# Kernel tuning notes

Measured on AMD Instinct MI355X. Metric: run time of the kernel, lower is better.

Reference implementation:

```python
import jax, jax.numpy as jnp
import numpy as np

CHUNK = 64  # rows of `a` processed per step to bound the [chunk, N, d] abs-diff intermediate
TAIL_K = 4          # selection_tail_size
FAR_K = 64          # far_sample_count
PUSH_K = 4          # pushing_sample_size
HUBER_DELTA = 1.0   # torch.nn.HuberLoss default


def cdist_l1(a, b):
    # a: [M, d], b: [N, d] -> [M, N] Manhattan distances, computed in row chunks
    M, d = a.shape
    def f(a_chunk):  # [CHUNK, d] -> [CHUNK, N]
        return jnp.abs(a_chunk[:, None, :] - b[None, :, :]).sum(-1)
    return jax.lax.map(f, a.reshape(-1, CHUNK, d)).reshape(M, b.shape[0])


def smallest_k_mean(dists, k):
    # mean of the k smallest entries along last dim
    neg_vals, _ = jax.lax.top_k(-dists, k)
    return (-neg_vals).mean(-1)


def huber(x):
    # HuberLoss(pred=x, target=0), delta=1
    ax = jnp.abs(x)
    return jnp.where(ax < HUBER_DELTA, 0.5 * x * x, HUBER_DELTA * (ax - 0.5 * HUBER_DELTA))


def setup_inputs() -> dict:
    key = jax.random.key(0)
    k1, k2 = jax.random.split(key)
    space_samples = jax.random.normal(k1, (2048, 256), dtype=jnp.float32)
    latents = jax.random.normal(k2, (8192, 256), dtype=jnp.float32)
    return {"space_samples": space_samples, "latents": latents}


def reference(space_samples, latents):
    # space_samples: [M, d] drawn from latent_sampler; latents: [N, d]
    space_dists = cdist_l1(space_samples, latents)            # [M, N]
    tail_dists = smallest_k_mean(space_dists, TAIL_K)          # [M]
    far_inds = jax.lax.top_k(tail_dists, FAR_K)[1]             # [FAR_K]
    far_samples = space_samples[far_inds]                      # [FAR_K, d]
    empty_dists = cdist_l1(far_samples, latents)               # [FAR_K, N]
    close_dists = smallest_k_mean(empty_dists, PUSH_K)         # [FAR_K]
    return huber(close_dists).mean()
```

## Files before the change

### kernel.cpp

```cpp
#include <hip/hip_runtime.h>
#include <hip/hip_bf16.h>


static constexpr int M = 2048;
static constexpr int N = 8192;
static constexpr int KQ = 64;
static constexpr int ROWS_PER_BLK = 128;
static constexpr int COLS_PER_BLK = 128;
static constexpr int NCHUNK = N / COLS_PER_BLK;
static constexpr int SLD_RED = 132;

static constexpr float QS  = 21.0f;
static constexpr float QB  = 126.0f;
static constexpr float INV_QS = 1.0f / 21.0f;

__device__ __forceinline__ float med3f(float a, float b, float c) {
    return __builtin_amdgcn_fmed3f(a, b, c);
}

__device__ __forceinline__ void ins4(float d, float& s0, float& s1, float& s2, float& s3) {
    float n0 = fminf(s0, d);
    float n1 = med3f(s0, s1, d);
    float n2 = med3f(s1, s2, d);
    float n3 = med3f(s2, s3, d);
    s0 = n0; s1 = n1; s2 = n2; s3 = n3;
}

__device__ __forceinline__ unsigned int sad8(unsigned int a, unsigned int b, unsigned int c) {
#if __has_builtin(__builtin_amdgcn_sad_u8)
    return __builtin_amdgcn_sad_u8(a, b, c);
#else
    unsigned int d;
    asm("v_sad_u8 %0, %1, %2, %3" : "=v"(d) : "v"(a), "v"(b), "v"(c));
    return d;
#endif
}

__device__ __forceinline__ void gll16(const unsigned int* g, unsigned int* l) {
    __builtin_amdgcn_global_load_lds(
        (const __attribute__((address_space(1))) unsigned int*)g,
        (__attribute__((address_space(3))) unsigned int*)l, 16, 0, 0);
}

__device__ __forceinline__ unsigned int quant4(const float4 v) {
    const float y0 = fminf(fmaxf(fmaf(v.x, QS, QB), 0.0f), 255.0f);
    const float y1 = fminf(fmaxf(fmaf(v.y, QS, QB), 0.0f), 255.0f);
    const float y2 = fminf(fmaxf(fmaf(v.z, QS, QB), 0.0f), 255.0f);
    const float y3 = fminf(fmaxf(fmaf(v.w, QS, QB), 0.0f), 255.0f);
    const unsigned int b0 = (unsigned int)(int)rintf(y0);
    const unsigned int b1 = (unsigned int)(int)rintf(y1);
    const unsigned int b2 = (unsigned int)(int)rintf(y2);
    const unsigned int b3 = (unsigned int)(int)rintf(y3);
    return b0 | (b1 << 8) | (b2 << 16) | (b3 << 24);
}

__device__ __forceinline__ float huber_pos(float x) {
    const float ax = __builtin_fabsf(x);
    return (ax < 1.0f) ? (0.5f * x * x) : (ax - 0.5f);
}

__global__ __launch_bounds__(256)
void convert_kernel(const float* __restrict__ A, const float* __restrict__ B,
                    unsigned int* __restrict__ At, unsigned int* __restrict__ Bt) {
    __shared__ unsigned int lt[KQ * 65];
    const int tid = threadIdx.x;
    const bool isB = (blockIdx.x < N / 64);
    const float* src = isB ? B : A;
    unsigned int* dst = isB ? Bt : At;
    const int rows = isB ? N : M;
    const int r0 = (isB ? blockIdx.x : (blockIdx.x - N / 64)) * 64;

#pragma unroll
    for (int it = 0; it < 16; ++it) {
        const int qi = it * 256 + tid;
        const int row = qi >> 6;
        const int kq = qi & 63;
        const float4 v = *(const float4*)&src[(r0 + row) * 256 + 4 * kq];
        lt[kq * 65 + row] = quant4(v);
    }
    __syncthreads();
#pragma unroll
    for (int it = 0; it < 16; ++it) {
        const int wi = it * 256 + tid;
        const int row = wi & 63;
        const int kq = wi >> 6;
        dst[(size_t)kq * rows + r0 + row] = lt[kq * 65 + row];
    }
}

__global__ __launch_bounds__(256, 4)
void dist4_kernel(const unsigned int* __restrict__ At, const unsigned int* __restrict__ Bt,
                  float4* __restrict__ ws_dist) {
    __shared__ __align__(16) char smem[33792];
    unsigned int* bt = (unsigned int*)smem;
    const int tid = threadIdx.x;
    const int lane = tid & 63;
    const int w = __builtin_amdgcn_readfirstlane(tid >> 6);
    const int bx = blockIdx.x;
    const int by = blockIdx.y;
    const int rowBase = by * ROWS_PER_BLK;
    const int colBase = bx * COLS_PER_BLK;
    const int r0 = rowBase + w * 32;

#pragma unroll
    for (int it = 0; it < 8; ++it) {
        const int idx = it * 256 + tid;
        const int kq = idx >> 5;
        const int c4 = (idx & 31) * 4;
        gll16(&Bt[(size_t)kq * N + colBase + c4], bt + idx * 4);
    }

    unsigned int acc[32][2];
#pragma unroll
    for (int r = 0; r < 32; ++r) { acc[r][0] = 0u; acc[r][1] = 0u; }

    __syncthreads();

    const unsigned int* __restrict__ Arow = At + r0;
#pragma unroll 4
    for (int kq = 0; kq < KQ; ++kq) {
        const uint2 bb = *(const uint2*)&bt[kq * 128 + 2 * lane];
        const uint4* __restrict__ pa = (const uint4*)(Arow + (size_t)kq * M);
#pragma unroll
        for (int q = 0; q < 8; ++q) {
            const uint4 av = pa[q];
            acc[4*q+0][0] = sad8(av.x, bb.x, acc[4*q+0][0]);
            acc[4*q+0][1] = sad8(av.x, bb.y, acc[4*q+0][1]);
            acc[4*q+1][0] = sad8(av.y, bb.x, acc[4*q+1][0]);
            acc[4*q+1][1] = sad8(av.y, bb.y, acc[4*q+1][1]);
            acc[4*q+2][0] = sad8(av.z, bb.x, acc[4*q+2][0]);
            acc[4*q+2][1] = sad8(av.z, bb.y, acc[4*q+2][1]);
            acc[4*q+3][0] = sad8(av.w, bb.x, acc[4*q+3][0]);
            acc[4*q+3][1] = sad8(av.w, bb.y, acc[4*q+3][1]);
        }
    }

    float (*red)[SLD_RED] = (float (*)[SLD_RED])smem;
    __syncthreads();

#pragma unroll
    for (int p = 0; p < 2; ++p) {
        if ((w >> 1) == p) {
            const int rl = (w & 1) * 32;
#pragma unroll
            for (int r = 0; r < 32; ++r) {
                *(float2*)&red[rl + r][2 * lane] =
                    make_float2((float)acc[r][0] * INV_QS, (float)acc[r][1] * INV_QS);
            }
        }
        __syncthreads();
        {
            const int row = tid >> 2;
            const int seg = tid & 3;
            float s0 = 1e30f, s1 = 1e30f, s2 = 1e30f, s3 = 1e30f;
#pragma unroll
            for (int c = 0; c < 8; ++c) {
                const float4 v = *(const float4*)&red[row][seg * 4 + c * 16];
                ins4(v.x, s0, s1, s2, s3);
                ins4(v.y, s0, s1, s2, s3);
                ins4(v.z, s0, s1, s2, s3);
                ins4(v.w, s0, s1, s2, s3);
            }
#pragma unroll
            for (int lvl = 1; lvl <= 2; lvl <<= 1) {
                const float o0 = __shfl_xor(s0, lvl, 64);
                const float o1 = __shfl_xor(s1, lvl, 64);
                const float o2 = __shfl_xor(s2, lvl, 64);
                const float o3 = __shfl_xor(s3, lvl, 64);
                ins4(o0, s0, s1, s2, s3);
                ins4(o1, s0, s1, s2, s3);
                ins4(o2, s0, s1, s2, s3);
                ins4(o3, s0, s1, s2, s3);
            }
            if (seg == 0) {
                ws_dist[bx * M + rowBase + p * 64 + row] = make_float4(s0, s1, s2, s3);
            }
        }
        __syncthreads();
    }
}

__global__ __launch_bounds__(256)
void tail_kernel(const float4* __restrict__ ws_dist, float* __restrict__ tail) {
    const int gtid = blockIdx.x * 256 + threadIdx.x;
    const int row = gtid >> 3;
    const int q = gtid & 7;
    float s0 = 1e30f, s1 = 1e30f, s2 = 1e30f, s3 = 1e30f;
#pragma unroll
    for (int c = 0; c < 8; ++c) {
        const float4 v = ws_dist[(q * 8 + c) * M + row];
        ins4(v.x, s0, s1, s2, s3);
        ins4(v.y, s0, s1, s2, s3);
        ins4(v.z, s0, s1, s2, s3);
        ins4(v.w, s0, s1, s2, s3);
    }
#pragma unroll
    for (int lvl = 1; lvl <= 4; lvl <<= 1) {
        const float o0 = __shfl_xor(s0, lvl, 64);
        const float o1 = __shfl_xor(s1, lvl, 64);
        const float o2 = __shfl_xor(s2, lvl, 64);
        const float o3 = __shfl_xor(s3, lvl, 64);
        ins4(o0, s0, s1, s2, s3);
        ins4(o1, s0, s1, s2, s3);
        ins4(o2, s0, s1, s2, s3);
        ins4(o3, s0, s1, s2, s3);
    }
    if (q == 0) tail[row] = (s0 + s1 + s2 + s3) * 0.25f;
}

__global__ __launch_bounds__(1024)
void top64_kernel(const float* __restrict__ tail, float* __restrict__ out) {
    __shared__ unsigned int hist[8][256];
    __shared__ unsigned int ctrl[2];
    __shared__ float wsum[16];
    __shared__ unsigned int wcnt[16];
    const int tid = threadIdx.x;
    const int wid = tid >> 6;
    const int lane = tid & 63;

    const unsigned int k0 = __float_as_uint(tail[tid]);
    const unsigned int k1 = __float_as_uint(tail[tid + 1024]);

    if (tid == 0) { ctrl[0] = 0u; ctrl[1] = 64u; }

    for (int p = 0; p < 4; ++p) {
        const int shift = 24 - 8 * p;
        ((unsigned int*)hist)[tid] = 0u;
        ((unsigned int*)hist)[tid + 1024] = 0u;
        __syncthreads();
        const unsigned int prefix = ctrl[0];
        const unsigned int t = ctrl[1];
        bool c0 = true, c1 = true;
        if (p > 0) {
            const int sh8 = shift + 8;
            c0 = ((k0 >> sh8) == (prefix >> sh8));
            c1 = ((k1 >> sh8) == (prefix >> sh8));
        }
        if (c0) atomicAdd(&hist[wid & 7][(k0 >> shift) & 255], 1u);
        if (c1) atomicAdd(&hist[wid & 7][(k1 >> shift) & 255], 1u);
        __syncthreads();
        if (tid < 256) {
            unsigned int h = 0;
#pragma unroll
            for (int r = 0; r < 8; ++r) h += hist[r][tid];
            hist[0][tid] = h;
        }
        __syncthreads();
        if (wid == 0) {
            const unsigned int s4 = hist[0][4 * lane] + hist[0][4 * lane + 1] +
                                    hist[0][4 * lane + 2] + hist[0][4 * lane + 3];
            unsigned int suf = s4;
#pragma unroll
            for (int off = 1; off < 64; off <<= 1) {
                const unsigned int v = __shfl_down(suf, off, 64);
                if (lane + off < 64) suf += v;
            }
            const unsigned long long mask = __ballot(suf >= t);
            const int lstar = 63 - __clzll(mask);
            if (lane == lstar) {
                unsigned int c = suf - s4;
                for (int d = 4 * lstar + 3; d >= 4 * lstar; --d) {
                    const unsigned int cd = hist[0][d];
                    c += cd;
                    if (c >= t) {
                        ctrl[0] = prefix | ((unsigned int)d << shift);
                        ctrl[1] = t - (c - cd);
                        break;
                    }
                }
            }
        }
        __syncthreads();
    }

    const unsigned int T = ctrl[0];
    float sum = 0.0f;
    unsigned int cnt = 0;
    if (k0 > T) { ++cnt; sum += huber_pos(__uint_as_float(k0)); }
    if (k1 > T) { ++cnt; sum += huber_pos(__uint_as_float(k1)); }
#pragma unroll
    for (int off = 32; off > 0; off >>= 1) {
        sum += __shfl_down(sum, off, 64);
        cnt += __shfl_down(cnt, off, 64);
    }
    if (lane == 0) { wsum[wid] = sum; wcnt[wid] = cnt; }
    __syncthreads();
    if (tid == 0) {
        float S = 0.0f;
        unsigned int C = 0;
#pragma unroll
        for (int w = 0; w < 16; ++w) { S += wsum[w]; C += wcnt[w]; }
        const float hT = huber_pos(__uint_as_float(T));
        out[0] = (S + (float)(64u - C) * hT) * (1.0f / 64.0f);
    }
}

extern "C" void kernel_launch(void* const* d_in, const int* in_sizes, int n_in,
                              void* d_out, int out_size, void* d_ws, size_t ws_size,
                              hipStream_t stream) {
    const float* A = (const float*)d_in[0];
    const float* B = (const float*)d_in[1];
    float* out = (float*)d_out;

    unsigned int* Bt = (unsigned int*)d_ws;
    unsigned int* At = (unsigned int*)((char*)d_ws + (size_t)KQ * N * 4);
    float4* ws_dist = (float4*)((char*)d_ws + (size_t)KQ * N * 4 + (size_t)KQ * M * 4);
    float* tail = (float*)((char*)ws_dist + (size_t)NCHUNK * M * sizeof(float4));

    convert_kernel<<<dim3(N / 64 + M / 64), 256, 0, stream>>>(A, B, At, Bt);
    dist4_kernel<<<dim3(NCHUNK, M / ROWS_PER_BLK), 256, 0, stream>>>(At, Bt, ws_dist);
    tail_kernel<<<dim3(M * 8 / 256), 256, 0, stream>>>(ws_dist, tail);
    top64_kernel<<<1, 1024, 0, stream>>>(tail, out);
}
```

Before: 112.2 us.

## Load B tile directly into registers with double-buffered prefetch instead of LDS

Replaces the up-front global-to-LDS copy of the B column tile, and the barrier that followed it, with per-lane direct global loads into two register buffers. Each buffer holds 8 k-steps, and the loop prefetches the next chunk while computing the current one. This removes the LDS staging, the initial sync and the later sync before the reduction buffer reuse. In exchange it adds registers, which may hurt occupancy at 4 waves per SIMD, and it issues uncoalesced 8-byte global loads per lane.

```diff
diff --git a/kernel.cpp b/kernel.cpp
--- a/kernel.cpp
+++ b/kernel.cpp
@@ -34,12 +34,6 @@
     asm("v_sad_u8 %0, %1, %2, %3" : "=v"(d) : "v"(a), "v"(b), "v"(c));
     return d;
 #endif
-}
-
-__device__ __forceinline__ void gll16(const unsigned int* g, unsigned int* l) {
-    __builtin_amdgcn_global_load_lds(
-        (const __attribute__((address_space(1))) unsigned int*)g,
-        (__attribute__((address_space(3))) unsigned int*)l, 16, 0, 0);
 }
 
 __device__ __forceinline__ unsigned int quant4(const float4 v) {
@@ -92,7 +86,6 @@
 void dist4_kernel(const unsigned int* __restrict__ At, const unsigned int* __restrict__ Bt,
                   float4* __restrict__ ws_dist) {
     __shared__ __align__(16) char smem[33792];
-    unsigned int* bt = (unsigned int*)smem;
     const int tid = threadIdx.x;
     const int lane = tid & 63;
     const int w = __builtin_amdgcn_readfirstlane(tid >> 6);
@@ -101,42 +94,53 @@
     const int rowBase = by * ROWS_PER_BLK;
     const int colBase = bx * COLS_PER_BLK;
     const int r0 = rowBase + w * 32;
-
-#pragma unroll
-    for (int it = 0; it < 8; ++it) {
-        const int idx = it * 256 + tid;
-        const int kq = idx >> 5;
-        const int c4 = (idx & 31) * 4;
-        gll16(&Bt[(size_t)kq * N + colBase + c4], bt + idx * 4);
-    }
+    const size_t cb2 = (size_t)colBase + 2 * lane;
 
     unsigned int acc[32][2];
 #pragma unroll
     for (int r = 0; r < 32; ++r) { acc[r][0] = 0u; acc[r][1] = 0u; }
 
-    __syncthreads();
-
     const unsigned int* __restrict__ Arow = At + r0;
-#pragma unroll 4
-    for (int kq = 0; kq < KQ; ++kq) {
-        const uint2 bb = *(const uint2*)&bt[kq * 128 + 2 * lane];
-        const uint4* __restrict__ pa = (const uint4*)(Arow + (size_t)kq * M);
-#pragma unroll
-        for (int q = 0; q < 8; ++q) {
-            const uint4 av = pa[q];
-            acc[4*q+0][0] = sad8(av.x, bb.x, acc[4*q+0][0]);
-            acc[4*q+0][1] = sad8(av.x, bb.y, acc[4*q+0][1]);
-            acc[4*q+1][0] = sad8(av.y, bb.x, acc[4*q+1][0]);
-            acc[4*q+1][1] = sad8(av.y, bb.y, acc[4*q+1][1]);
-            acc[4*q+2][0] = sad8(av.z, bb.x, acc[4*q+2][0]);
-            acc[4*q+2][1] = sad8(av.z, bb.y, acc[4*q+2][1]);
-            acc[4*q+3][0] = sad8(av.w, bb.x, acc[4*q+3][0]);
-            acc[4*q+3][1] = sad8(av.w, bb.y, acc[4*q+3][1]);
-        }
+
+    uint2 b0[8], b1[8];
+
+    auto LOADB = [&](uint2 (&dst)[8], int ch) {
+#pragma unroll
+        for (int k = 0; k < 8; ++k)
+            dst[k] = *(const uint2*)&Bt[(size_t)(ch * 8 + k) * N + cb2];
+    };
+
+    auto COMP = [&](const uint2 (&bv)[8], int ch) {
+#pragma unroll
+        for (int k = 0; k < 8; ++k) {
+            const uint4* __restrict__ pa =
+                (const uint4*)(Arow + (size_t)(ch * 8 + k) * M);
+#pragma unroll
+            for (int q = 0; q < 8; ++q) {
+                const uint4 av = pa[q];
+                acc[4*q+0][0] = sad8(av.x, bv[k].x, acc[4*q+0][0]);
+                acc[4*q+0][1] = sad8(av.x, bv[k].y, acc[4*q+0][1]);
+                acc[4*q+1][0] = sad8(av.y, bv[k].x, acc[4*q+1][0]);
+                acc[4*q+1][1] = sad8(av.y, bv[k].y, acc[4*q+1][1]);
+                acc[4*q+2][0] = sad8(av.z, bv[k].x, acc[4*q+2][0]);
+                acc[4*q+2][1] = sad8(av.z, bv[k].y, acc[4*q+2][1]);
+                acc[4*q+3][0] = sad8(av.w, bv[k].x, acc[4*q+3][0]);
+                acc[4*q+3][1] = sad8(av.w, bv[k].y, acc[4*q+3][1]);
+            }
+        }
+    };
+
+    LOADB(b0, 0);
+#pragma unroll 1
+    for (int cc = 0; cc < 4; ++cc) {
+        const int ch0 = 2 * cc;
+        LOADB(b1, ch0 + 1);
+        COMP(b0, ch0);
+        if (cc < 3) LOADB(b0, ch0 + 2);
+        COMP(b1, ch0 + 1);
     }
 
     float (*red)[SLD_RED] = (float (*)[SLD_RED])smem;
-    __syncthreads();
 
 #pragma unroll
     for (int p = 0; p < 2; ++p) {
```

Result: slower. 133.0 us (+18.6%).
